# Performance work log

Hardware: AMD Instinct MI355X
Metric: run time of the kernel (lower is better)

Reference implementation:

```python
import jax, jax.numpy as jnp
import numpy as np

EMBEDDING_DIM = 1024

def _pe_table(seq_len, dim, dtype):
    pos = jnp.arange(seq_len, dtype=jnp.float32)[:, None]        # [S,1]
    i = jnp.arange(dim)                                          # [D]
    k = (i // 2).astype(jnp.float32)                             # i//2 per source
    # NOTE: source uses exponent k/dim (not 2k/dim) -- faithful to the code
    angle = pos / jnp.power(10000.0, k / dim)                    # [S,D]
    pe = jnp.where((i % 2) == 0, jnp.sin(angle), jnp.cos(angle))
    return pe.astype(dtype)


def setup_inputs() -> dict:
    key = jax.random.key(0)
    x = jax.random.normal(key, (8, 4096, EMBEDDING_DIM), dtype=jnp.float32)
    return {"x": x}


def reference(x) -> jnp.ndarray:
    B, S, D = x.shape
    pe = _pe_table(S, D, x.dtype)          # [S,D]
    return x + pe[None, :, :]              # broadcast over batch
```

## Files before the change

### kernel.cpp

```cpp
#include <hip/hip_runtime.h>


#define PE_B 8
#define PE_S 4096
#define PE_D 1024
#define ROW4 (PE_S * PE_D / 4)

typedef float v4f __attribute__((ext_vector_type(4)));

__global__ __launch_bounds__(256) void pe_table_kernel(v4f* __restrict__ pe_tab) {
    const int tid = blockIdx.x * blockDim.x + threadIdx.x;
    const int i   = (tid & (PE_D / 4 - 1)) * 4;
    const int s   = tid >> 8;

    const float pos = (float)s;
    const float c   = -13.287712379549449f / (float)PE_D;
    const float k0  = (float)(i >> 1);
    const float a0  = pos * exp2f(k0 * c);
    const float a1  = pos * exp2f((k0 + 1.0f) * c);
    float s0, c0, s1, c1;
    sincosf(a0, &s0, &c0);
    sincosf(a1, &s1, &c1);
    const v4f pe = {s0, c0, s1, c1};
    pe_tab[tid] = pe;
}

__global__ __launch_bounds__(256) void pe_add_kernel(
    const float* __restrict__ x, const v4f* __restrict__ pe_tab,
    float* __restrict__ out) {
    const int idx = blockIdx.x * blockDim.x + threadIdx.x;
    const v4f v = *(const v4f*)(x + (size_t)idx * 4);
    const v4f p = pe_tab[idx & (ROW4 - 1)];
    *(v4f*)(out + (size_t)idx * 4) = v + p;
}

__global__ __launch_bounds__(256) void pe_fused_kernel(
    const float* __restrict__ x, float* __restrict__ out) {
    const int idx = blockIdx.x * blockDim.x + threadIdx.x;
    const int r   = idx & (ROW4 - 1);
    const int i   = (r & (PE_D / 4 - 1)) * 4;
    const int s   = r >> 8;

    const v4f v = *(const v4f*)(x + (size_t)idx * 4);

    const float pos = (float)s;
    const float c   = -13.287712379549449f / (float)PE_D;
    const float k0  = (float)(i >> 1);
    const float a0  = pos * exp2f(k0 * c);
    const float a1  = pos * exp2f((k0 + 1.0f) * c);
    float s0, c0, s1, c1;
    sincosf(a0, &s0, &c0);
    sincosf(a1, &s1, &c1);
    const v4f pe = {s0, c0, s1, c1};
    *(v4f*)(out + (size_t)idx * 4) = v + pe;
}

extern "C" void kernel_launch(void* const* d_in, const int* in_sizes, int n_in,
                              void* d_out, int out_size, void* d_ws, size_t ws_size,
                              hipStream_t stream) {
    const float* x = (const float*)d_in[0];
    float* out = (float*)d_out;
    const int n4 = PE_B * ROW4;

    if (ws_size >= (size_t)PE_S * PE_D * sizeof(float)) {
        v4f* pe_tab = (v4f*)d_ws;
        pe_table_kernel<<<ROW4 / 256, 256, 0, stream>>>(pe_tab);
        pe_add_kernel<<<n4 / 256, 256, 0, stream>>>(x, pe_tab, out);
    } else {
        pe_fused_kernel<<<n4 / 256, 256, 0, stream>>>(x, out);
    }
}
```

Baseline: 228.7 us.

## Fuse PE table into add kernel, computing each PE value once per batch loop

Replaces the two-kernel scheme (PE table write, then broadcast add) with a single kernel. Each thread computes one PE vector and applies it to all 8 batch rows, with the 8 loads issued up front. This removes the 16 MB table write and its re-reads plus a launch, and cuts the transcendental work by a factor of 8 compared with the old fused path. The cost is an 8x smaller grid and more registers per thread, which may reduce occupancy and how many memory requests are in flight.

New measurement: 239.3 us. +4.6%, slower.

```diff
diff --git a/kernel.cpp b/kernel.cpp
--- a/kernel.cpp
+++ b/kernel.cpp
@@ -5,13 +5,21 @@
 #define PE_S 4096
 #define PE_D 1024
 #define ROW4 (PE_S * PE_D / 4)
+#define ROWF ((size_t)PE_S * PE_D)
 
 typedef float v4f __attribute__((ext_vector_type(4)));
 
-__global__ __launch_bounds__(256) void pe_table_kernel(v4f* __restrict__ pe_tab) {
-    const int tid = blockIdx.x * blockDim.x + threadIdx.x;
-    const int i   = (tid & (PE_D / 4 - 1)) * 4;
-    const int s   = tid >> 8;
+__global__ __launch_bounds__(256) void pe_fused_amortized(
+    const float* __restrict__ x, float* __restrict__ out) {
+    const int r = blockIdx.x * blockDim.x + threadIdx.x;
+    const int i = (r & (PE_D / 4 - 1)) * 4;
+    const int s = r >> 8;
+
+    const float* xp = x + (size_t)r * 4;
+    v4f xv[PE_B];
+#pragma unroll
+    for (int b = 0; b < PE_B; ++b)
+        xv[b] = *(const v4f*)(xp + (size_t)b * ROWF);
 
     const float pos = (float)s;
     const float c   = -13.287712379549449f / (float)PE_D;
@@ -22,37 +30,11 @@
     sincosf(a0, &s0, &c0);
     sincosf(a1, &s1, &c1);
     const v4f pe = {s0, c0, s1, c1};
-    pe_tab[tid] = pe;
-}
 
-__global__ __launch_bounds__(256) void pe_add_kernel(
-    const float* __restrict__ x, const v4f* __restrict__ pe_tab,
-    float* __restrict__ out) {
-    const int idx = blockIdx.x * blockDim.x + threadIdx.x;
-    const v4f v = *(const v4f*)(x + (size_t)idx * 4);
-    const v4f p = pe_tab[idx & (ROW4 - 1)];
-    *(v4f*)(out + (size_t)idx * 4) = v + p;
-}
-
-__global__ __launch_bounds__(256) void pe_fused_kernel(
-    const float* __restrict__ x, float* __restrict__ out) {
-    const int idx = blockIdx.x * blockDim.x + threadIdx.x;
-    const int r   = idx & (ROW4 - 1);
-    const int i   = (r & (PE_D / 4 - 1)) * 4;
-    const int s   = r >> 8;
-
-    const v4f v = *(const v4f*)(x + (size_t)idx * 4);
-
-    const float pos = (float)s;
-    const float c   = -13.287712379549449f / (float)PE_D;
-    const float k0  = (float)(i >> 1);
-    const float a0  = pos * exp2f(k0 * c);
-    const float a1  = pos * exp2f((k0 + 1.0f) * c);
-    float s0, c0, s1, c1;
-    sincosf(a0, &s0, &c0);
-    sincosf(a1, &s1, &c1);
-    const v4f pe = {s0, c0, s1, c1};
-    *(v4f*)(out + (size_t)idx * 4) = v + pe;
+    float* op = out + (size_t)r * 4;
+#pragma unroll
+    for (int b = 0; b < PE_B; ++b)
+        *(v4f*)(op + (size_t)b * ROWF) = xv[b] + pe;
 }
 
 extern "C" void kernel_launch(void* const* d_in, const int* in_sizes, int n_in,
@@ -60,13 +42,6 @@
                               hipStream_t stream) {
     const float* x = (const float*)d_in[0];
     float* out = (float*)d_out;
-    const int n4 = PE_B * ROW4;
-
-    if (ws_size >= (size_t)PE_S * PE_D * sizeof(float)) {
-        v4f* pe_tab = (v4f*)d_ws;
-        pe_table_kernel<<<ROW4 / 256, 256, 0, stream>>>(pe_tab);
-        pe_add_kernel<<<n4 / 256, 256, 0, stream>>>(x, pe_tab, out);
-    } else {
-        pe_fused_kernel<<<n4 / 256, 256, 0, stream>>>(x, out);
-    }
+    (void)d_ws; (void)ws_size;
+    pe_fused_amortized<<<ROW4 / 256, 256, 0, stream>>>(x, out);
 }
```
